# Kernel tuning notes

Hardware: AMD Instinct MI355X
Metric: run time of the kernel (lower is better)

The kernel has to match this reference:

```python
import jax, jax.numpy as jnp
import numpy as np

N_NODES = 50000
N_EDGES = 800000
D = 64
B = 64
HL = 128  # lstm hidden
OUT = 32


def setup_inputs() -> dict:
    key = jax.random.key(0)
    ks = jax.random.split(key, 16)
    s = 0.05
    return {
        "x": jax.random.normal(ks[0], (N_NODES, D), jnp.float32),
        "edge_index": jax.random.randint(ks[1], (2, N_EDGES), 0, N_NODES),
        "batch": jnp.sort(jax.random.randint(ks[2], (N_NODES,), 0, B)),
        "w1": jax.random.normal(ks[3], (D, D), jnp.float32) * s,
        "b1": jnp.zeros((D,), jnp.float32),
        "w2": jax.random.normal(ks[4], (D, D), jnp.float32) * s,
        "b2": jnp.zeros((D,), jnp.float32),
        "w3": jax.random.normal(ks[5], (D, D), jnp.float32) * s,
        "b3": jnp.zeros((D,), jnp.float32),
        "w4": jax.random.normal(ks[6], (D, D), jnp.float32) * s,
        "b4": jnp.zeros((D,), jnp.float32),
        "w_ih": jax.random.normal(ks[7], (4 * HL, D), jnp.float32) * s,
        "w_hh": jax.random.normal(ks[8], (4 * HL, HL), jnp.float32) * s,
        "b_ih": jnp.zeros((4 * HL,), jnp.float32),
        "b_hh": jnp.zeros((4 * HL,), jnp.float32),
        "fc_w": jax.random.normal(ks[9], (OUT, HL), jnp.float32) * s,
        "fc_b": jnp.zeros((OUT,), jnp.float32),
        "h0": jax.random.normal(ks[10], (1, B, HL), jnp.float32),
        "c0": jax.random.normal(ks[11], (1, B, HL), jnp.float32),
    }


def _gin(x, edge_index, wA, bA, wB, bB):
    # GINConv with eps=0: MLP(x + sum_{j->i} x_j); scatter-add over edges
    agg = jax.ops.segment_sum(x[edge_index[0]], edge_index[1], num_segments=N_NODES)
    h = x + agg
    h = jax.nn.relu(h @ wA.T + bA)
    return h @ wB.T + bB


def reference(x, edge_index, batch, w1, b1, w2, b2, w3, b3, w4, b4,
              w_ih, w_hh, b_ih, b_hh, fc_w, fc_b, h0, c0):
    h = jax.nn.relu(_gin(x, edge_index, w1, b1, w2, b2))  # dropout = identity (eval)
    h = jax.nn.relu(_gin(h, edge_index, w3, b3, w4, b4))
    # global_mean_pool over graphs
    sums = jax.ops.segment_sum(h, batch, num_segments=B)              # [B, D]
    cnts = jax.ops.segment_sum(jnp.ones((N_NODES,), h.dtype), batch, num_segments=B)
    pooled = sums / jnp.maximum(cnts, 1.0)[:, None]
    # single-step LSTM (PyTorch gate order: i, f, g, o)
    gates = pooled @ w_ih.T + b_ih + h0[0] @ w_hh.T + b_hh            # [B, 4H]
    i, f, g, o = jnp.split(gates, 4, axis=-1)
    c1 = jax.nn.sigmoid(f) * c0[0] + jax.nn.sigmoid(i) * jnp.tanh(g)
    h1 = jax.nn.sigmoid(o) * jnp.tanh(c1)
    logits = h1 @ fc_w.T + fc_b
    probs = jax.nn.softmax(logits, axis=1)
    return probs, h1[None], c1[None]
```

## Files before the change

kernel.cpp:

```cpp
#include <hip/hip_runtime.h>
#include <hip/hip_bf16.h>

#define N_NODES 50000
#define N_EDGES 800000
#define D 64
#define B 64
#define HL 128
#define OUT 32

#define CAP 64
#define STP 72
#define ZROW N_NODES

#define BINS 196
#define EPB 2048
#define LCAP 48
#define BCAP 4608

#define AB 391
#define CB 3125
#define MB 782

typedef __attribute__((ext_vector_type(8))) short          short8;
typedef __attribute__((ext_vector_type(8))) unsigned short ushort8_t;
typedef __attribute__((ext_vector_type(4))) float          floatx4;

__device__ __forceinline__ unsigned short f2bf(float f)
{
    unsigned u = __float_as_uint(f);
    u = (u + 0x7FFFu + ((u >> 16) & 1u)) >> 16;
    return (unsigned short)u;
}
__device__ __forceinline__ float bf2f(unsigned short s)
{
    return __uint_as_float(((unsigned)s) << 16);
}
__device__ __forceinline__ float bfLO(unsigned u) { return __uint_as_float(u << 16); }
__device__ __forceinline__ float bfHI(unsigned u) { return __uint_as_float(u & 0xffff0000u); }

__global__ __launch_bounds__(256) void fused_pro_kernel(
    const int*   __restrict__ ei,
    int*         __restrict__ bincnt,
    unsigned*    __restrict__ binbuf,
    const float* __restrict__ x, unsigned short* __restrict__ xb,
    const float* __restrict__ w1, const float* __restrict__ w2,
    const float* __restrict__ w3, const float* __restrict__ w4,
    unsigned short* __restrict__ wb,
    unsigned short* __restrict__ h1,
    float*       __restrict__ psum)
{
    __shared__ int      lcnt[BINS];
    __shared__ int      gbase[BINS];
    __shared__ unsigned lbuf[BINS * LCAP];

    int t = threadIdx.x;

    if (blockIdx.x < AB) {
        if (t < BINS) lcnt[t] = 0;
        __syncthreads();

        int base = blockIdx.x * EPB;
#pragma unroll
        for (int i = 0; i < EPB / 256; ++i) {
            int e = base + i * 256 + t;
            if (e < N_EDGES) {
                int s = ei[e];
                int d = ei[N_EDGES + e];
                int bin = d >> 8;
                unsigned pk = (unsigned)s | ((unsigned)(d & 255) << 16);
                int p = atomicAdd(&lcnt[bin], 1);
                if (p < LCAP) {
                    lbuf[bin * LCAP + p] = pk;
                } else {
                    int q = atomicAdd(&bincnt[bin], 1);
                    if (q < BCAP) binbuf[bin * BCAP + q] = pk;
                }
            }
        }
        __syncthreads();

        if (t < BINS) {
            int m = lcnt[t]; m = (m < LCAP) ? m : LCAP;
            gbase[t] = (m > 0) ? atomicAdd(&bincnt[t], m) : 0;
        }
        __syncthreads();

        int wv = t >> 6, lane = t & 63;
        for (int b = wv; b < BINS; b += 4) {
            int m = lcnt[b]; m = (m < LCAP) ? m : LCAP;
            int gb = gbase[b];
            for (int j = lane; j < m; j += 64)
                if (gb + j < BCAP) binbuf[b * BCAP + gb + j] = lbuf[b * LCAP + j];
        }
    } else if (blockIdx.x < AB + CB) {
        int cb = blockIdx.x - AB;
        int i = cb * 256 + t;
        const float4 v = reinterpret_cast<const float4*>(x)[i];
        ushort4 o;
        o.x = f2bf(v.x); o.y = f2bf(v.y); o.z = f2bf(v.z); o.w = f2bf(v.w);
        reinterpret_cast<ushort4*>(xb)[i] = o;

        if (cb < 64) {
            int j = cb * 256 + t;
            int m = j >> 12, off = j & 4095;
            const float* src = (m == 0) ? w1 : (m == 1) ? w2 : (m == 2) ? w3 : w4;
            wb[j] = f2bf(src[off]);
        }
    } else {
        if (t < D) {
            xb[(size_t)ZROW * D + t] = 0;
            h1[(size_t)ZROW * D + t] = 0;
        }
#pragma unroll
        for (int k = 0; k < 16; ++k)
            psum[t * 16 + k] = 0.0f;
    }
}

__device__ __forceinline__ void build_bucket64(
    const int*      __restrict__ bincnt,
    const unsigned* __restrict__ binbuf,
    unsigned short* lbkt,
    int*            lc,
    int bn0, int t)
{
    {
        ushort8_t fill = {ZROW, ZROW, ZROW, ZROW, ZROW, ZROW, ZROW, ZROW};
        reinterpret_cast<ushort8_t*>(lbkt)[t]       = fill;
        reinterpret_cast<ushort8_t*>(lbkt)[t + 256] = fill;
    }
    if (t < 64) lc[t] = 0;
    __syncthreads();

    const int bin = bn0 >> 8;
    const int q   = (bn0 >> 6) & 3;
    int m = bincnt[bin]; m = (m < BCAP) ? m : BCAP;
    const unsigned* src = binbuf + bin * BCAP;
    for (int j = t; j < m; j += 256) {
        unsigned pk = src[j];
        int dlow = (pk >> 16) & 255;
        if ((dlow >> 6) == q) {
            int r = dlow & 63;
            int p = atomicAdd(&lc[r], 1);
            if (p < CAP) lbkt[r * CAP + p] = (unsigned short)(pk & 0xFFFFu);
        }
    }
    __syncthreads();
}

__device__ __forceinline__ void gather16_lds(
    const unsigned short* __restrict__ feat,
    const unsigned short* lbkt,
    const int*            lc,
    unsigned short*       stw,
    int bn0, int wv, int lane)
{
    const int g = lane >> 4;
    const int c = lane & 15;

#pragma unroll
    for (int b = 0; b < 4; ++b) {
        const int rloc = wv * 16 + b * 4 + g;
        const int node = bn0 + rloc;
        int deg = lc[rloc];
        deg = (deg < CAP) ? deg : CAP;
        int m = (deg + 7) >> 3;
        {
            int t1 = __shfl_xor(m, 16); m = (t1 > m) ? t1 : m;
            int t2 = __shfl_xor(m, 32); m = (t2 > m) ? t2 : m;
        }

        const unsigned short* bkt = lbkt + rloc * CAP;

        uint2 u = *reinterpret_cast<const uint2*>(feat + (size_t)node * D + 4 * c);
        float a0 = bfLO(u.x), a1 = bfHI(u.x);
        float a2 = bfLO(u.y), a3 = bfHI(u.y);

        ushort8_t idx = *reinterpret_cast<const ushort8_t*>(bkt);
        for (int r = 0; r < m; ++r) {
            ushort8_t nxt = *reinterpret_cast<const ushort8_t*>(bkt + (r + 1) * 8);
#pragma unroll
            for (int j = 0; j < 8; ++j) {
                uint2 v = *reinterpret_cast<const uint2*>(
                    feat + (size_t)idx[j] * D + 4 * c);
                a0 += bfLO(v.x); a1 += bfHI(v.x);
                a2 += bfLO(v.y); a3 += bfHI(v.y);
            }
            idx = nxt;
        }

        uint2 o;
        o.x = (unsigned)f2bf(a0) | ((unsigned)f2bf(a1) << 16);
        o.y = (unsigned)f2bf(a2) | ((unsigned)f2bf(a3) << 16);
        *reinterpret_cast<uint2*>(stw + (b * 4 + g) * STP + 4 * c) = o;
    }
}

__global__ __launch_bounds__(256) void gmlp_kernel(
    const unsigned short* __restrict__ feat,
    const int*            __restrict__ bincnt,
    const unsigned*       __restrict__ binbuf,
    const unsigned short* __restrict__ wAb,
    const float*          __restrict__ bA,
    const unsigned short* __restrict__ wBb,
    const float*          __restrict__ bB,
    unsigned short*       __restrict__ outp)
{
    __shared__ int lc[64];
    __shared__ __align__(16) unsigned short lbkt[64 * CAP + 16];
    __shared__ __align__(16) unsigned short st[4][16 * STP];

    const int t    = threadIdx.x;
    const int wv   = t >> 6;
    const int lane = t & 63;
    const int quad = lane >> 4;
    const int col  = lane & 15;

    const int bn0 = blockIdx.x * 64;
    const int n0  = bn0 + wv * 16;

    build_bucket64(bincnt, binbuf, lbkt, lc, bn0, t);

    if (n0 >= N_NODES) return;

    float bAl[4], bBl[4];
#pragma unroll
    for (int tt = 0; tt < 4; ++tt) {
        bAl[tt] = bA[tt * 16 + col];
        bBl[tt] = bB[tt * 16 + col];
    }

    short8 WA[4][2], WB[4][2];
#pragma unroll
    for (int tt = 0; tt < 4; ++tt)
#pragma unroll
        for (int k = 0; k < 2; ++k) {
            WA[tt][k] = *reinterpret_cast<const short8*>(
                wAb + (tt * 16 + col) * D + k * 32 + quad * 8);
            WB[tt][k] = *reinterpret_cast<const short8*>(
                wBb + (tt * 16 + col) * D + k * 32 + quad * 8);
        }

    unsigned short* stw = &st[wv][0];

    gather16_lds(feat, lbkt, lc, stw, bn0, wv, lane);

    short8 A0 = *reinterpret_cast<const short8*>(stw + col * STP + 0 * 32 + quad * 8);
    short8 A1 = *reinterpret_cast<const short8*>(stw + col * STP + 1 * 32 + quad * 8);

#pragma unroll
    for (int tt = 0; tt < 4; ++tt) {
        floatx4 c = {0.0f, 0.0f, 0.0f, 0.0f};
        c = __builtin_amdgcn_mfma_f32_16x16x32_bf16(A0, WA[tt][0], c, 0, 0, 0);
        c = __builtin_amdgcn_mfma_f32_16x16x32_bf16(A1, WA[tt][1], c, 0, 0, 0);
#pragma unroll
        for (int r = 0; r < 4; ++r) {
            float v = fmaxf(c[r] + bAl[tt], 0.0f);
            stw[(quad * 4 + r) * STP + tt * 16 + col] = f2bf(v);
        }
    }

    short8 T0 = *reinterpret_cast<const short8*>(stw + col * STP + 0 * 32 + quad * 8);
    short8 T1 = *reinterpret_cast<const short8*>(stw + col * STP + 1 * 32 + quad * 8);

#pragma unroll
    for (int tt = 0; tt < 4; ++tt) {
        floatx4 c = {0.0f, 0.0f, 0.0f, 0.0f};
        c = __builtin_amdgcn_mfma_f32_16x16x32_bf16(T0, WB[tt][0], c, 0, 0, 0);
        c = __builtin_amdgcn_mfma_f32_16x16x32_bf16(T1, WB[tt][1], c, 0, 0, 0);
#pragma unroll
        for (int r = 0; r < 4; ++r) {
            float v = fmaxf(c[r] + bBl[tt], 0.0f);
            outp[(size_t)(n0 + quad * 4 + r) * D + tt * 16 + col] = f2bf(v);
        }
    }
}

__global__ __launch_bounds__(256) void g2mlp_pool_kernel(
    const unsigned short* __restrict__ feat,
    const int*            __restrict__ bincnt,
    const unsigned*       __restrict__ binbuf,
    const unsigned short* __restrict__ wAb,
    const float*          __restrict__ bA,
    const unsigned short* __restrict__ wBb,
    const float*          __restrict__ bB,
    const int*            __restrict__ batch,
    float*                __restrict__ psum)
{
    __shared__ int lc[64];
    __shared__ __align__(16) unsigned short lbkt[64 * CAP + 16];
    __shared__ __align__(16) unsigned short st[4][16 * STP];
    __shared__ float pt[64][D + 1];
    __shared__ int   sbatch[64];

    const int t    = threadIdx.x;
    const int wv   = t >> 6;
    const int lane = t & 63;
    const int quad = lane >> 4;
    const int col  = lane & 15;

    const int bn0 = blockIdx.x * 64;
    const int n0  = bn0 + wv * 16;
    const bool active = (n0 < N_NODES);

    if (t < 64) {
        int n = bn0 + t;
        sbatch[t] = (n < N_NODES) ? batch[n] : -1;
    }

    build_bucket64(bincnt, binbuf, lbkt, lc, bn0, t);

    if (active) {
        float bAl[4], bBl[4];
#pragma unroll
        for (int tt = 0; tt < 4; ++tt) {
            bAl[tt] = bA[tt * 16 + col];
            bBl[tt] = bB[tt * 16 + col];
        }

        short8 WA[4][2], WB[4][2];
#pragma unroll
        for (int tt = 0; tt < 4; ++tt)
#pragma unroll
            for (int k = 0; k < 2; ++k) {
                WA[tt][k] = *reinterpret_cast<const short8*>(
                    wAb + (tt * 16 + col) * D + k * 32 + quad * 8);
                WB[tt][k] = *reinterpret_cast<const short8*>(
                    wBb + (tt * 16 + col) * D + k * 32 + quad * 8);
            }

        unsigned short* stw = &st[wv][0];

        gather16_lds(feat, lbkt, lc, stw, bn0, wv, lane);

        short8 A0 = *reinterpret_cast<const short8*>(stw + col * STP + 0 * 32 + quad * 8);
        short8 A1 = *reinterpret_cast<const short8*>(stw + col * STP + 1 * 32 + quad * 8);

#pragma unroll
        for (int tt = 0; tt < 4; ++tt) {
            floatx4 c = {0.0f, 0.0f, 0.0f, 0.0f};
            c = __builtin_amdgcn_mfma_f32_16x16x32_bf16(A0, WA[tt][0], c, 0, 0, 0);
            c = __builtin_amdgcn_mfma_f32_16x16x32_bf16(A1, WA[tt][1], c, 0, 0, 0);
#pragma unroll
            for (int r = 0; r < 4; ++r) {
                float v = fmaxf(c[r] + bAl[tt], 0.0f);
                stw[(quad * 4 + r) * STP + tt * 16 + col] = f2bf(v);
            }
        }

        short8 T0 = *reinterpret_cast<const short8*>(stw + col * STP + 0 * 32 + quad * 8);
        short8 T1 = *reinterpret_cast<const short8*>(stw + col * STP + 1 * 32 + quad * 8);

#pragma unroll
        for (int tt = 0; tt < 4; ++tt) {
            floatx4 c = {0.0f, 0.0f, 0.0f, 0.0f};
            c = __builtin_amdgcn_mfma_f32_16x16x32_bf16(T0, WB[tt][0], c, 0, 0, 0);
            c = __builtin_amdgcn_mfma_f32_16x16x32_bf16(T1, WB[tt][1], c, 0, 0, 0);
#pragma unroll
            for (int r = 0; r < 4; ++r) {
                float v = fmaxf(c[r] + bBl[tt], 0.0f);
                pt[wv * 16 + quad * 4 + r][tt * 16 + col] = v;
            }
        }
    } else {
        for (int c2 = 0; c2 < 4; ++c2)
#pragma unroll
            for (int r = 0; r < 4; ++r)
                pt[wv * 16 + quad * 4 + r][c2 * 16 + col] = 0.0f;
    }
    __syncthreads();

    int q = t >> 6;
    int d = t & 63;
    float acc = 0.0f;
    int curg = sbatch[q * 16];
#pragma unroll
    for (int r = 0; r < 16; ++r) {
        int row = q * 16 + r;
        int g2 = sbatch[row];
        float v = pt[row][d];
        if (g2 != curg) {
            if (curg >= 0) atomicAdd(&psum[curg * D + d], acc);
            acc = 0.0f;
            curg = g2;
        }
        acc += v;
    }
    if (curg >= 0) atomicAdd(&psum[curg * D + d], acc);
}

__device__ __forceinline__ int lower_bound_dev(const int* a, int n, int v)
{
    int lo = 0, hi = n;
    while (lo < hi) {
        int m = (lo + hi) >> 1;
        if (a[m] < v) lo = m + 1; else hi = m;
    }
    return lo;
}

__device__ __forceinline__ float sigmoidf_(float x) { return 1.0f / (1.0f + expf(-x)); }

__global__ __launch_bounds__(512) void head_kernel(
    const float* __restrict__ psum,
    const int*   __restrict__ batch,
    const float* __restrict__ w_ih,
    const float* __restrict__ w_hh,
    const float* __restrict__ b_ih,
    const float* __restrict__ b_hh,
    const float* __restrict__ fc_w,
    const float* __restrict__ fc_b,
    const float* __restrict__ h0,
    const float* __restrict__ c0,
    float*       __restrict__ out_probs,
    float*       __restrict__ out_h1,
    float*       __restrict__ out_c1)
{
    int b = blockIdx.x;
    int j = threadIdx.x;

    __shared__ float sp[D];
    __shared__ float sh[HL];
    __shared__ float gates[4 * HL];
    __shared__ float sh1[HL];
    __shared__ float slog[OUT];

    if (j < D) {
        int start = lower_bound_dev(batch, N_NODES, b);
        int end   = lower_bound_dev(batch, N_NODES, b + 1);
        sp[j] = psum[b * D + j] / fmaxf((float)(end - start), 1.0f);
    } else if (j < D + HL) {
        sh[j - D] = h0[b * HL + (j - D)];
    }
    __syncthreads();

    {
        float acc = b_ih[j] + b_hh[j];
#pragma unroll
        for (int k = 0; k < D; ++k)  acc = fmaf(sp[k], w_ih[j * D + k], acc);
#pragma unroll
        for (int k = 0; k < HL; ++k) acc = fmaf(sh[k], w_hh[j * HL + k], acc);
        gates[j] = acc;
    }
    __syncthreads();

    if (j < HL) {
        float ig = gates[j];
        float fg = gates[HL + j];
        float gg = gates[2 * HL + j];
        float og = gates[3 * HL + j];
        float c  = sigmoidf_(fg) * c0[b * HL + j] + sigmoidf_(ig) * tanhf(gg);
        float hv = sigmoidf_(og) * tanhf(c);
        out_c1[b * HL + j] = c;
        out_h1[b * HL + j] = hv;
        sh1[j] = hv;
    }
    __syncthreads();

    if (j < OUT) {
        float a = fc_b[j];
#pragma unroll
        for (int k = 0; k < HL; ++k) a = fmaf(sh1[k], fc_w[j * HL + k], a);
        slog[j] = a;
    }
    __syncthreads();

    if (j < OUT) {
        float m = -1e30f;
#pragma unroll
        for (int k = 0; k < OUT; ++k) m = fmaxf(m, slog[k]);
        float s = 0.0f;
#pragma unroll
        for (int k = 0; k < OUT; ++k) s += expf(slog[k] - m);
        out_probs[b * OUT + j] = expf(slog[j] - m) / s;
    }
}

extern "C" void kernel_launch(void* const* d_in, const int* in_sizes, int n_in,
                              void* d_out, int out_size, void* d_ws, size_t ws_size,
                              hipStream_t stream)
{
    const float* x     = (const float*)d_in[0];
    const int*   ei    = (const int*)  d_in[1];
    const int*   batch = (const int*)  d_in[2];
    const float* w1    = (const float*)d_in[3];
    const float* b1    = (const float*)d_in[4];
    const float* w2    = (const float*)d_in[5];
    const float* b2    = (const float*)d_in[6];
    const float* w3    = (const float*)d_in[7];
    const float* b3    = (const float*)d_in[8];
    const float* w4    = (const float*)d_in[9];
    const float* b4    = (const float*)d_in[10];
    const float* w_ih  = (const float*)d_in[11];
    const float* w_hh  = (const float*)d_in[12];
    const float* b_ih  = (const float*)d_in[13];
    const float* b_hh  = (const float*)d_in[14];
    const float* fc_w  = (const float*)d_in[15];
    const float* fc_b  = (const float*)d_in[16];
    const float* h0    = (const float*)d_in[17];
    const float* c0    = (const float*)d_in[18];

    const size_t NR = (size_t)N_NODES + 16;
    int* bincnt = (int*)d_ws;
    unsigned* binbuf = (unsigned*)(bincnt + 256);
    unsigned short* xb = (unsigned short*)(binbuf + (size_t)BINS * BCAP);
    unsigned short* h1 = xb + NR * D;
    unsigned short* wb = h1 + NR * D;
    float* psum = (float*)(wb + 4 * D * D);

    float* out_probs = (float*)d_out;
    float* out_h1    = out_probs + B * OUT;
    float* out_c1    = out_h1 + B * HL;

    hipMemsetAsync(bincnt, 0, 256 * sizeof(int), stream);
    fused_pro_kernel<<<AB + CB + 1, 256, 0, stream>>>(
        ei, bincnt, binbuf, x, xb, w1, w2, w3, w4, wb, h1, psum);

    gmlp_kernel<<<MB, 256, 0, stream>>>(xb, bincnt, binbuf,
                                        wb, b1, wb + 4096, b2, h1);

    g2mlp_pool_kernel<<<MB, 256, 0, stream>>>(h1, bincnt, binbuf,
                                              wb + 8192, b3, wb + 12288, b4,
                                              batch, psum);

    head_kernel<<<B, 512, 0, stream>>>(psum, batch, w_ih, w_hh, b_ih, b_hh,
                                       fc_w, fc_b, h0, c0,
                                       out_probs, out_h1, out_c1);
}
```

Before: 199.0 us.

## Gather fp32 x directly in first GIN layer, drop bf16 conversion pass

Removes the x-to-bf16 conversion blocks from the prologue, so the first gather reads fp32 rows of x directly and masks padded indices instead of using a zero row. Binning blocks now process 8192 edges each with a larger local cap, and weights are converted by four dedicated blocks. Per-graph node counts are accumulated during pooling, which replaces the binary searches over batch in the head kernel. The trade-off is that the first gather moves twice the bytes per neighbor, in exchange for skipping a full pass over x and the extra prologue blocks.

```diff
diff --git a/kernel.cpp b/kernel.cpp
--- a/kernel.cpp
+++ b/kernel.cpp
@@ -13,12 +13,11 @@
 #define ZROW N_NODES
 
 #define BINS 196
-#define EPB 2048
-#define LCAP 48
+#define EPB 8192
+#define LCAP 76
 #define BCAP 4608
 
-#define AB 391
-#define CB 3125
+#define AB 98
 #define MB 782
 
 typedef __attribute__((ext_vector_type(8))) short          short8;
@@ -31,23 +30,19 @@
     u = (u + 0x7FFFu + ((u >> 16) & 1u)) >> 16;
     return (unsigned short)u;
 }
-__device__ __forceinline__ float bf2f(unsigned short s)
-{
-    return __uint_as_float(((unsigned)s) << 16);
-}
 __device__ __forceinline__ float bfLO(unsigned u) { return __uint_as_float(u << 16); }
 __device__ __forceinline__ float bfHI(unsigned u) { return __uint_as_float(u & 0xffff0000u); }
 
-__global__ __launch_bounds__(256) void fused_pro_kernel(
+__global__ __launch_bounds__(256) void pro_kernel(
     const int*   __restrict__ ei,
     int*         __restrict__ bincnt,
     unsigned*    __restrict__ binbuf,
-    const float* __restrict__ x, unsigned short* __restrict__ xb,
     const float* __restrict__ w1, const float* __restrict__ w2,
     const float* __restrict__ w3, const float* __restrict__ w4,
     unsigned short* __restrict__ wb,
     unsigned short* __restrict__ h1,
-    float*       __restrict__ psum)
+    float*       __restrict__ psum,
+    float*       __restrict__ cnts)
 {
     __shared__ int      lcnt[BINS];
     __shared__ int      gbase[BINS];
@@ -60,7 +55,7 @@
         __syncthreads();
 
         int base = blockIdx.x * EPB;
-#pragma unroll
+#pragma unroll 8
         for (int i = 0; i < EPB / 256; ++i) {
             int e = base + i * 256 + t;
             if (e < N_EDGES) {
@@ -92,28 +87,20 @@
             for (int j = lane; j < m; j += 64)
                 if (gb + j < BCAP) binbuf[b * BCAP + gb + j] = lbuf[b * LCAP + j];
         }
-    } else if (blockIdx.x < AB + CB) {
-        int cb = blockIdx.x - AB;
-        int i = cb * 256 + t;
-        const float4 v = reinterpret_cast<const float4*>(x)[i];
-        ushort4 o;
-        o.x = f2bf(v.x); o.y = f2bf(v.y); o.z = f2bf(v.z); o.w = f2bf(v.w);
-        reinterpret_cast<ushort4*>(xb)[i] = o;
-
-        if (cb < 64) {
-            int j = cb * 256 + t;
-            int m = j >> 12, off = j & 4095;
-            const float* src = (m == 0) ? w1 : (m == 1) ? w2 : (m == 2) ? w3 : w4;
-            wb[j] = f2bf(src[off]);
+    } else if (blockIdx.x < AB + 4) {
+        int m = blockIdx.x - AB;
+        const float* src = (m == 0) ? w1 : (m == 1) ? w2 : (m == 2) ? w3 : w4;
+#pragma unroll
+        for (int k = 0; k < 16; ++k) {
+            int off = k * 256 + t;
+            wb[m * 4096 + off] = f2bf(src[off]);
         }
     } else {
-        if (t < D) {
-            xb[(size_t)ZROW * D + t] = 0;
-            h1[(size_t)ZROW * D + t] = 0;
-        }
+        if (t < D) h1[(size_t)ZROW * D + t] = 0;
 #pragma unroll
         for (int k = 0; k < 16; ++k)
             psum[t * 16 + k] = 0.0f;
+        if (t < B) cnts[t] = 0.0f;
     }
 }
 
@@ -148,8 +135,8 @@
     __syncthreads();
 }
 
-__device__ __forceinline__ void gather16_lds(
-    const unsigned short* __restrict__ feat,
+__device__ __forceinline__ void gather16_f32(
+    const float*          __restrict__ x,
     const unsigned short* lbkt,
     const int*            lc,
     unsigned short*       stw,
@@ -172,6 +159,58 @@
 
         const unsigned short* bkt = lbkt + rloc * CAP;
 
+        float4 u = *reinterpret_cast<const float4*>(x + (size_t)node * D + 4 * c);
+        float a0 = u.x, a1 = u.y, a2 = u.z, a3 = u.w;
+
+        ushort8_t idx = *reinterpret_cast<const ushort8_t*>(bkt);
+        for (int r = 0; r < m; ++r) {
+            ushort8_t nxt = *reinterpret_cast<const ushort8_t*>(bkt + (r + 1) * 8);
+#pragma unroll
+            for (int j = 0; j < 8; ++j) {
+                int id = idx[j];
+                float msk = (id < N_NODES) ? 1.0f : 0.0f;
+                int id2   = (id < N_NODES) ? id : 0;
+                float4 v = *reinterpret_cast<const float4*>(
+                    x + (size_t)id2 * D + 4 * c);
+                a0 = fmaf(v.x, msk, a0);
+                a1 = fmaf(v.y, msk, a1);
+                a2 = fmaf(v.z, msk, a2);
+                a3 = fmaf(v.w, msk, a3);
+            }
+            idx = nxt;
+        }
+
+        uint2 o;
+        o.x = (unsigned)f2bf(a0) | ((unsigned)f2bf(a1) << 16);
+        o.y = (unsigned)f2bf(a2) | ((unsigned)f2bf(a3) << 16);
+        *reinterpret_cast<uint2*>(stw + (b * 4 + g) * STP + 4 * c) = o;
+    }
+}
+
+__device__ __forceinline__ void gather16_bf16(
+    const unsigned short* __restrict__ feat,
+    const unsigned short* lbkt,
+    const int*            lc,
+    unsigned short*       stw,
+    int bn0, int wv, int lane)
+{
+    const int g = lane >> 4;
+    const int c = lane & 15;
+
+#pragma unroll
+    for (int b = 0; b < 4; ++b) {
+        const int rloc = wv * 16 + b * 4 + g;
+        const int node = bn0 + rloc;
+        int deg = lc[rloc];
+        deg = (deg < CAP) ? deg : CAP;
+        int m = (deg + 7) >> 3;
+        {
+            int t1 = __shfl_xor(m, 16); m = (t1 > m) ? t1 : m;
+            int t2 = __shfl_xor(m, 32); m = (t2 > m) ? t2 : m;
+        }
+
+        const unsigned short* bkt = lbkt + rloc * CAP;
+
         uint2 u = *reinterpret_cast<const uint2*>(feat + (size_t)node * D + 4 * c);
         float a0 = bfLO(u.x), a1 = bfHI(u.x);
         float a2 = bfLO(u.y), a3 = bfHI(u.y);
@@ -197,7 +236,7 @@
 }
 
 __global__ __launch_bounds__(256) void gmlp_kernel(
-    const unsigned short* __restrict__ feat,
+    const float*          __restrict__ x,
     const int*            __restrict__ bincnt,
     const unsigned*       __restrict__ binbuf,
     const unsigned short* __restrict__ wAb,
@@ -243,7 +282,7 @@
 
     unsigned short* stw = &st[wv][0];
 
-    gather16_lds(feat, lbkt, lc, stw, bn0, wv, lane);
+    gather16_f32(x, lbkt, lc, stw, bn0, wv, lane);
 
     short8 A0 = *reinterpret_cast<const short8*>(stw + col * STP + 0 * 32 + quad * 8);
     short8 A1 = *reinterpret_cast<const short8*>(stw + col * STP + 1 * 32 + quad * 8);
@@ -285,7 +324,8 @@
     const unsigned short* __restrict__ wBb,
     const float*          __restrict__ bB,
     const int*            __restrict__ batch,
-    float*                __restrict__ psum)
+    float*                __restrict__ psum,
+    float*                __restrict__ cnts)
 {
     __shared__ int lc[64];
     __shared__ __align__(16) unsigned short lbkt[64 * CAP + 16];
@@ -331,7 +371,7 @@
 
         unsigned short* stw = &st[wv][0];
 
-        gather16_lds(feat, lbkt, lc, stw, bn0, wv, lane);
+        gather16_bf16(feat, lbkt, lc, stw, bn0, wv, lane);
 
         short8 A0 = *reinterpret_cast<const short8*>(stw + col * STP + 0 * 32 + quad * 8);
         short8 A1 = *reinterpret_cast<const short8*>(stw + col * STP + 1 * 32 + quad * 8);
@@ -373,6 +413,7 @@
     int q = t >> 6;
     int d = t & 63;
     float acc = 0.0f;
+    int   len = 0;
     int curg = sbatch[q * 16];
 #pragma unroll
     for (int r = 0; r < 16; ++r) {
@@ -380,30 +421,27 @@
         int g2 = sbatch[row];
         float v = pt[row][d];
         if (g2 != curg) {
-            if (curg >= 0) atomicAdd(&psum[curg * D + d], acc);
-            acc = 0.0f;
+            if (curg >= 0) {
+                atomicAdd(&psum[curg * D + d], acc);
+                if (d == 0) atomicAdd(&cnts[curg], (float)len);
+            }
+            acc = 0.0f; len = 0;
             curg = g2;
         }
         acc += v;
-    }
-    if (curg >= 0) atomicAdd(&psum[curg * D + d], acc);
-}
-
-__device__ __forceinline__ int lower_bound_dev(const int* a, int n, int v)
-{
-    int lo = 0, hi = n;
-    while (lo < hi) {
-        int m = (lo + hi) >> 1;
-        if (a[m] < v) lo = m + 1; else hi = m;
-    }
-    return lo;
+        len += 1;
+    }
+    if (curg >= 0) {
+        atomicAdd(&psum[curg * D + d], acc);
+        if (d == 0) atomicAdd(&cnts[curg], (float)len);
+    }
 }
 
 __device__ __forceinline__ float sigmoidf_(float x) { return 1.0f / (1.0f + expf(-x)); }
 
 __global__ __launch_bounds__(512) void head_kernel(
     const float* __restrict__ psum,
-    const int*   __restrict__ batch,
+    const float* __restrict__ cnts,
     const float* __restrict__ w_ih,
     const float* __restrict__ w_hh,
     const float* __restrict__ b_ih,
@@ -426,9 +464,7 @@
     __shared__ float slog[OUT];
 
     if (j < D) {
-        int start = lower_bound_dev(batch, N_NODES, b);
-        int end   = lower_bound_dev(batch, N_NODES, b + 1);
-        sp[j] = psum[b * D + j] / fmaxf((float)(end - start), 1.0f);
+        sp[j] = psum[b * D + j] / fmaxf(cnts[b], 1.0f);
     } else if (j < D + HL) {
         sh[j - D] = h0[b * HL + (j - D)];
     }
@@ -503,27 +539,27 @@
     const size_t NR = (size_t)N_NODES + 16;
     int* bincnt = (int*)d_ws;
     unsigned* binbuf = (unsigned*)(bincnt + 256);
-    unsigned short* xb = (unsigned short*)(binbuf + (size_t)BINS * BCAP);
-    unsigned short* h1 = xb + NR * D;
+    unsigned short* h1 = (unsigned short*)(binbuf + (size_t)BINS * BCAP);
     unsigned short* wb = h1 + NR * D;
     float* psum = (float*)(wb + 4 * D * D);
+    float* cnts = psum + B * D;
 
     float* out_probs = (float*)d_out;
     float* out_h1    = out_probs + B * OUT;
     float* out_c1    = out_h1 + B * HL;
 
     hipMemsetAsync(bincnt, 0, 256 * sizeof(int), stream);
-    fused_pro_kernel<<<AB + CB + 1, 256, 0, stream>>>(
-        ei, bincnt, binbuf, x, xb, w1, w2, w3, w4, wb, h1, psum);
-
-    gmlp_kernel<<<MB, 256, 0, stream>>>(xb, bincnt, binbuf,
+    pro_kernel<<<AB + 5, 256, 0, stream>>>(
+        ei, bincnt, binbuf, w1, w2, w3, w4, wb, h1, psum, cnts);
+
+    gmlp_kernel<<<MB, 256, 0, stream>>>(x, bincnt, binbuf,
                                         wb, b1, wb + 4096, b2, h1);
 
     g2mlp_pool_kernel<<<MB, 256, 0, stream>>>(h1, bincnt, binbuf,
                                               wb + 8192, b3, wb + 12288, b4,
-                                              batch, psum);
-
-    head_kernel<<<B, 512, 0, stream>>>(psum, batch, w_ih, w_hh, b_ih, b_hh,
+                                              batch, psum, cnts);
+
+    head_kernel<<<B, 512, 0, stream>>>(psum, cnts, w_ih, w_hh, b_ih, b_hh,
                                        fc_w, fc_b, h0, c0,
                                        out_probs, out_h1, out_c1);
 }
```

New measurement: 232.7 us. 1.17x slower.

## Use 512-thread blocks for neighbor gather and accumulate graph counts during pooling

Applied to the files above, without the earlier changes.

The two GIN MLP kernels now launch 512 threads per block. Eight waves each gather 8 rows of neighbor sums into shared memory, then four waves run the MFMA MLP on the staged tiles after a barrier. The goal is more memory-level parallelism in the latency-bound gather. Separately, per-graph node counts are accumulated with atomics in the pooling step, replacing two binary searches over the batch array per block in the head kernel. The price is an extra block barrier, idle waves during the MLP phase, and a few more atomics.

```diff
diff --git a/kernel.cpp b/kernel.cpp
--- a/kernel.cpp
+++ b/kernel.cpp
@@ -31,14 +31,10 @@
     u = (u + 0x7FFFu + ((u >> 16) & 1u)) >> 16;
     return (unsigned short)u;
 }
-__device__ __forceinline__ float bf2f(unsigned short s)
-{
-    return __uint_as_float(((unsigned)s) << 16);
-}
 __device__ __forceinline__ float bfLO(unsigned u) { return __uint_as_float(u << 16); }
 __device__ __forceinline__ float bfHI(unsigned u) { return __uint_as_float(u & 0xffff0000u); }
 
-__global__ __launch_bounds__(256) void fused_pro_kernel(
+__global__ __launch_bounds__(256) void pro_kernel(
     const int*   __restrict__ ei,
     int*         __restrict__ bincnt,
     unsigned*    __restrict__ binbuf,
@@ -47,7 +43,8 @@
     const float* __restrict__ w3, const float* __restrict__ w4,
     unsigned short* __restrict__ wb,
     unsigned short* __restrict__ h1,
-    float*       __restrict__ psum)
+    float*       __restrict__ psum,
+    float*       __restrict__ cnts)
 {
     __shared__ int      lcnt[BINS];
     __shared__ int      gbase[BINS];
@@ -114,6 +111,7 @@
 #pragma unroll
         for (int k = 0; k < 16; ++k)
             psum[t * 16 + k] = 0.0f;
+        if (t < B) cnts[t] = 0.0f;
     }
 }
 
@@ -126,8 +124,8 @@
 {
     {
         ushort8_t fill = {ZROW, ZROW, ZROW, ZROW, ZROW, ZROW, ZROW, ZROW};
-        reinterpret_cast<ushort8_t*>(lbkt)[t]       = fill;
-        reinterpret_cast<ushort8_t*>(lbkt)[t + 256] = fill;
+        for (int i = t; i < (64 * CAP + 16) / 8; i += 512)
+            reinterpret_cast<ushort8_t*>(lbkt)[i] = fill;
     }
     if (t < 64) lc[t] = 0;
     __syncthreads();
@@ -136,7 +134,7 @@
     const int q   = (bn0 >> 6) & 3;
     int m = bincnt[bin]; m = (m < BCAP) ? m : BCAP;
     const unsigned* src = binbuf + bin * BCAP;
-    for (int j = t; j < m; j += 256) {
+    for (int j = t; j < m; j += 512) {
         unsigned pk = src[j];
         int dlow = (pk >> 16) & 255;
         if ((dlow >> 6) == q) {
@@ -148,19 +146,19 @@
     __syncthreads();
 }
 
-__device__ __forceinline__ void gather16_lds(
+__device__ __forceinline__ void gather8_bf16(
     const unsigned short* __restrict__ feat,
     const unsigned short* lbkt,
     const int*            lc,
-    unsigned short*       stw,
+    unsigned short*       stbase,
     int bn0, int wv, int lane)
 {
     const int g = lane >> 4;
     const int c = lane & 15;
 
 #pragma unroll
-    for (int b = 0; b < 4; ++b) {
-        const int rloc = wv * 16 + b * 4 + g;
+    for (int b = 0; b < 2; ++b) {
+        const int rloc = wv * 8 + b * 4 + g;
         const int node = bn0 + rloc;
         int deg = lc[rloc];
         deg = (deg < CAP) ? deg : CAP;
@@ -189,14 +187,16 @@
             idx = nxt;
         }
 
+        const int tile = wv >> 1;
+        const int row  = (wv & 1) * 8 + b * 4 + g;
         uint2 o;
         o.x = (unsigned)f2bf(a0) | ((unsigned)f2bf(a1) << 16);
         o.y = (unsigned)f2bf(a2) | ((unsigned)f2bf(a3) << 16);
-        *reinterpret_cast<uint2*>(stw + (b * 4 + g) * STP + 4 * c) = o;
-    }
-}
-
-__global__ __launch_bounds__(256) void gmlp_kernel(
+        *reinterpret_cast<uint2*>(stbase + (tile * 16 + row) * STP + 4 * c) = o;
+    }
+}
+
+__global__ __launch_bounds__(512) void gmlp_kernel(
     const unsigned short* __restrict__ feat,
     const int*            __restrict__ bincnt,
     const unsigned*       __restrict__ binbuf,
@@ -217,10 +217,15 @@
     const int col  = lane & 15;
 
     const int bn0 = blockIdx.x * 64;
-    const int n0  = bn0 + wv * 16;
 
     build_bucket64(bincnt, binbuf, lbkt, lc, bn0, t);
 
+    if (bn0 + wv * 8 < N_NODES)
+        gather8_bf16(feat, lbkt, lc, &st[0][0], bn0, wv, lane);
+    __syncthreads();
+
+    if (wv >= 4) return;
+    const int n0 = bn0 + wv * 16;
     if (n0 >= N_NODES) return;
 
     float bAl[4], bBl[4];
@@ -243,8 +248,6 @@
 
     unsigned short* stw = &st[wv][0];
 
-    gather16_lds(feat, lbkt, lc, stw, bn0, wv, lane);
-
     short8 A0 = *reinterpret_cast<const short8*>(stw + col * STP + 0 * 32 + quad * 8);
     short8 A1 = *reinterpret_cast<const short8*>(stw + col * STP + 1 * 32 + quad * 8);
 
@@ -276,7 +279,7 @@
     }
 }
 
-__global__ __launch_bounds__(256) void g2mlp_pool_kernel(
+__global__ __launch_bounds__(512) void g2mlp_pool_kernel(
     const unsigned short* __restrict__ feat,
     const int*            __restrict__ bincnt,
     const unsigned*       __restrict__ binbuf,
@@ -285,7 +288,8 @@
     const unsigned short* __restrict__ wBb,
     const float*          __restrict__ bB,
     const int*            __restrict__ batch,
-    float*                __restrict__ psum)
+    float*                __restrict__ psum,
+    float*                __restrict__ cnts)
 {
     __shared__ int lc[64];
     __shared__ __align__(16) unsigned short lbkt[64 * CAP + 16];
@@ -300,8 +304,6 @@
     const int col  = lane & 15;
 
     const int bn0 = blockIdx.x * 64;
-    const int n0  = bn0 + wv * 16;
-    const bool active = (n0 < N_NODES);
 
     if (t < 64) {
         int n = bn0 + t;
@@ -310,100 +312,105 @@
 
     build_bucket64(bincnt, binbuf, lbkt, lc, bn0, t);
 
-    if (active) {
-        float bAl[4], bBl[4];
-#pragma unroll
-        for (int tt = 0; tt < 4; ++tt) {
-            bAl[tt] = bA[tt * 16 + col];
-            bBl[tt] = bB[tt * 16 + col];
-        }
-
-        short8 WA[4][2], WB[4][2];
-#pragma unroll
-        for (int tt = 0; tt < 4; ++tt)
-#pragma unroll
-            for (int k = 0; k < 2; ++k) {
-                WA[tt][k] = *reinterpret_cast<const short8*>(
-                    wAb + (tt * 16 + col) * D + k * 32 + quad * 8);
-                WB[tt][k] = *reinterpret_cast<const short8*>(
-                    wBb + (tt * 16 + col) * D + k * 32 + quad * 8);
+    if (bn0 + wv * 8 < N_NODES)
+        gather8_bf16(feat, lbkt, lc, &st[0][0], bn0, wv, lane);
+    __syncthreads();
+
+    if (wv < 4) {
+        const int n0 = bn0 + wv * 16;
+        if (n0 < N_NODES) {
+            float bAl[4], bBl[4];
+#pragma unroll
+            for (int tt = 0; tt < 4; ++tt) {
+                bAl[tt] = bA[tt * 16 + col];
+                bBl[tt] = bB[tt * 16 + col];
             }
 
-        unsigned short* stw = &st[wv][0];
-
-        gather16_lds(feat, lbkt, lc, stw, bn0, wv, lane);
-
-        short8 A0 = *reinterpret_cast<const short8*>(stw + col * STP + 0 * 32 + quad * 8);
-        short8 A1 = *reinterpret_cast<const short8*>(stw + col * STP + 1 * 32 + quad * 8);
-
-#pragma unroll
-        for (int tt = 0; tt < 4; ++tt) {
-            floatx4 c = {0.0f, 0.0f, 0.0f, 0.0f};
-            c = __builtin_amdgcn_mfma_f32_16x16x32_bf16(A0, WA[tt][0], c, 0, 0, 0);
-            c = __builtin_amdgcn_mfma_f32_16x16x32_bf16(A1, WA[tt][1], c, 0, 0, 0);
-#pragma unroll
-            for (int r = 0; r < 4; ++r) {
-                float v = fmaxf(c[r] + bAl[tt], 0.0f);
-                stw[(quad * 4 + r) * STP + tt * 16 + col] = f2bf(v);
+            short8 WA[4][2], WB[4][2];
+#pragma unroll
+            for (int tt = 0; tt < 4; ++tt)
+#pragma unroll
+                for (int k = 0; k < 2; ++k) {
+                    WA[tt][k] = *reinterpret_cast<const short8*>(
+                        wAb + (tt * 16 + col) * D + k * 32 + quad * 8);
+                    WB[tt][k] = *reinterpret_cast<const short8*>(
+                        wBb + (tt * 16 + col) * D + k * 32 + quad * 8);
+                }
+
+            unsigned short* stw = &st[wv][0];
+
+            short8 A0 = *reinterpret_cast<const short8*>(stw + col * STP + 0 * 32 + quad * 8);
+            short8 A1 = *reinterpret_cast<const short8*>(stw + col * STP + 1 * 32 + quad * 8);
+
+#pragma unroll
+            for (int tt = 0; tt < 4; ++tt) {
+                floatx4 c = {0.0f, 0.0f, 0.0f, 0.0f};
+                c = __builtin_amdgcn_mfma_f32_16x16x32_bf16(A0, WA[tt][0], c, 0, 0, 0);
+                c = __builtin_amdgcn_mfma_f32_16x16x32_bf16(A1, WA[tt][1], c, 0, 0, 0);
+#pragma unroll
+                for (int r = 0; r < 4; ++r) {
+                    float v = fmaxf(c[r] + bAl[tt], 0.0f);
+                    stw[(quad * 4 + r) * STP + tt * 16 + col] = f2bf(v);
+                }
             }
-        }
-
-        short8 T0 = *reinterpret_cast<const short8*>(stw + col * STP + 0 * 32 + quad * 8);
-        short8 T1 = *reinterpret_cast<const short8*>(stw + col * STP + 1 * 32 + quad * 8);
-
-#pragma unroll
-        for (int tt = 0; tt < 4; ++tt) {
-            floatx4 c = {0.0f, 0.0f, 0.0f, 0.0f};
-            c = __builtin_amdgcn_mfma_f32_16x16x32_bf16(T0, WB[tt][0], c, 0, 0, 0);
-            c = __builtin_amdgcn_mfma_f32_16x16x32_bf16(T1, WB[tt][1], c, 0, 0, 0);
-#pragma unroll
-            for (int r = 0; r < 4; ++r) {
-                float v = fmaxf(c[r] + bBl[tt], 0.0f);
-                pt[wv * 16 + quad * 4 + r][tt * 16 + col] = v;
+
+            short8 T0 = *reinterpret_cast<const short8*>(stw + col * STP + 0 * 32 + quad * 8);
+            short8 T1 = *reinterpret_cast<const short8*>(stw + col * STP + 1 * 32 + quad * 8);
+
+#pragma unroll
+            for (int tt = 0; tt < 4; ++tt) {
+                floatx4 c = {0.0f, 0.0f, 0.0f, 0.0f};
+                c = __builtin_amdgcn_mfma_f32_16x16x32_bf16(T0, WB[tt][0], c, 0, 0, 0);
+                c = __builtin_amdgcn_mfma_f32_16x16x32_bf16(T1, WB[tt][1], c, 0, 0, 0);
+#pragma unroll
+                for (int r = 0; r < 4; ++r) {
+                    float v = fmaxf(c[r] + bBl[tt], 0.0f);
+                    pt[wv * 16 + quad * 4 + r][tt * 16 + col] = v;
+                }
             }
-        }
-    } else {
-        for (int c2 = 0; c2 < 4; ++c2)
-#pragma unroll
-            for (int r = 0; r < 4; ++r)
-                pt[wv * 16 + quad * 4 + r][c2 * 16 + col] = 0.0f;
-    }
-    __syncthreads();
-
-    int q = t >> 6;
-    int d = t & 63;
-    float acc = 0.0f;
-    int curg = sbatch[q * 16];
-#pragma unroll
-    for (int r = 0; r < 16; ++r) {
-        int row = q * 16 + r;
-        int g2 = sbatch[row];
-        float v = pt[row][d];
-        if (g2 != curg) {
-            if (curg >= 0) atomicAdd(&psum[curg * D + d], acc);
-            acc = 0.0f;
-            curg = g2;
-        }
-        acc += v;
-    }
-    if (curg >= 0) atomicAdd(&psum[curg * D + d], acc);
-}
-
-__device__ __forceinline__ int lower_bound_dev(const int* a, int n, int v)
-{
-    int lo = 0, hi = n;
-    while (lo < hi) {
-        int m = (lo + hi) >> 1;
-        if (a[m] < v) lo = m + 1; else hi = m;
-    }
-    return lo;
+        } else {
+            for (int c2 = 0; c2 < 4; ++c2)
+#pragma unroll
+                for (int r = 0; r < 4; ++r)
+                    pt[wv * 16 + quad * 4 + r][c2 * 16 + col] = 0.0f;
+        }
+    }
+    __syncthreads();
+
+    if (t < 256) {
+        int q = t >> 6;
+        int d = t & 63;
+        float acc = 0.0f;
+        int   len = 0;
+        int curg = sbatch[q * 16];
+#pragma unroll
+        for (int r = 0; r < 16; ++r) {
+            int row = q * 16 + r;
+            int g2 = sbatch[row];
+            float v = pt[row][d];
+            if (g2 != curg) {
+                if (curg >= 0) {
+                    atomicAdd(&psum[curg * D + d], acc);
+                    if (d == 0) atomicAdd(&cnts[curg], (float)len);
+                }
+                acc = 0.0f; len = 0;
+                curg = g2;
+            }
+            acc += v;
+            len += 1;
+        }
+        if (curg >= 0) {
+            atomicAdd(&psum[curg * D + d], acc);
+            if (d == 0) atomicAdd(&cnts[curg], (float)len);
+        }
+    }
 }
 
 __device__ __forceinline__ float sigmoidf_(float x) { return 1.0f / (1.0f + expf(-x)); }
 
 __global__ __launch_bounds__(512) void head_kernel(
     const float* __restrict__ psum,
-    const int*   __restrict__ batch,
+    const float* __restrict__ cnts,
     const float* __restrict__ w_ih,
     const float* __restrict__ w_hh,
     const float* __restrict__ b_ih,
@@ -426,9 +433,7 @@
     __shared__ float slog[OUT];
 
     if (j < D) {
-        int start = lower_bound_dev(batch, N_NODES, b);
-        int end   = lower_bound_dev(batch, N_NODES, b + 1);
-        sp[j] = psum[b * D + j] / fmaxf((float)(end - start), 1.0f);
+        sp[j] = psum[b * D + j] / fmaxf(cnts[b], 1.0f);
     } else if (j < D + HL) {
         sh[j - D] = h0[b * HL + (j - D)];
     }
@@ -507,23 +512,24 @@
     unsigned short* h1 = xb + NR * D;
     unsigned short* wb = h1 + NR * D;
     float* psum = (float*)(wb + 4 * D * D);
+    float* cnts = psum + B * D;
 
     float* out_probs = (float*)d_out;
     float* out_h1    = out_probs + B * OUT;
     float* out_c1    = out_h1 + B * HL;
 
     hipMemsetAsync(bincnt, 0, 256 * sizeof(int), stream);
-    fused_pro_kernel<<<AB + CB + 1, 256, 0, stream>>>(
-        ei, bincnt, binbuf, x, xb, w1, w2, w3, w4, wb, h1, psum);
-
-    gmlp_kernel<<<MB, 256, 0, stream>>>(xb, bincnt, binbuf,
+    pro_kernel<<<AB + CB + 1, 256, 0, stream>>>(
+        ei, bincnt, binbuf, x, xb, w1, w2, w3, w4, wb, h1, psum, cnts);
+
+    gmlp_kernel<<<MB, 512, 0, stream>>>(xb, bincnt, binbuf,
                                         wb, b1, wb + 4096, b2, h1);
 
-    g2mlp_pool_kernel<<<MB, 256, 0, stream>>>(h1, bincnt, binbuf,
+    g2mlp_pool_kernel<<<MB, 512, 0, stream>>>(h1, bincnt, binbuf,
                                               wb + 8192, b3, wb + 12288, b4,
-                                              batch, psum);
-
-    head_kernel<<<B, 512, 0, stream>>>(psum, batch, w_ih, w_hh, b_ih, b_hh,
+                                              batch, psum, cnts);
+
+    head_kernel<<<B, 512, 0, stream>>>(psum, cnts, w_ih, w_hh, b_ih, b_hh,
                                        fc_w, fc_b, h0, c0,
                                        out_probs, out_h1, out_c1);
 }
```

Result: slower. 209.4 us (+5.2%).
